# Optimization experiments

Hardware: AMD Instinct MI355X
Metric: run time of the kernel (lower is better)

Reference implementation:

```python
import jax, jax.numpy as jnp
import numpy as np
from jax import lax

BN_EPS = 1e-5

def _tern(w):
    # TWN-style ternarization with straight-through estimator
    d = 0.7 * jnp.mean(jnp.abs(w))
    q = jnp.where(jnp.abs(w) > d, jnp.sign(w), jnp.zeros_like(w))
    return w + lax.stop_gradient(q - w)

def _conv(x, w, b):
    y = lax.conv_general_dilated(x, _tern(w), (1, 1), 'SAME',
                                 dimension_numbers=('NCHW', 'OIHW', 'NCHW'))
    return y + b[None, :, None, None]

def _bn4(x, g, b, m, v):
    inv = g * lax.rsqrt(v + BN_EPS)
    return (x - m[None, :, None, None]) * inv[None, :, None, None] + b[None, :, None, None]

def _bn2(x, g, b, m, v):
    return (x - m) * (g * lax.rsqrt(v + BN_EPS)) + b

def _pool(x):
    return lax.reduce_window(x, -jnp.inf, lax.max, (1, 1, 2, 2), (1, 1, 2, 2), 'VALID')


def setup_inputs() -> dict:
    key = jax.random.key(0)
    ks = jax.random.split(key, 8)
    f = jnp.float32
    d = {}
    d['x'] = jax.random.normal(ks[0], (1024, 1, 28, 28), f)
    wshapes = {'w1': (32, 1, 3, 3), 'w2': (64, 32, 3, 3), 'w3': (128, 64, 3, 3),
               'w4': (128, 128, 3, 3), 'wf1': (256, 6272), 'wf2': (128, 256), 'wf3': (10, 128)}
    for i, (n, s) in enumerate(wshapes.items()):
        d[n] = jax.random.normal(ks[i + 1], s, f) * 0.1
    for n, c in [('1', 32), ('2', 64), ('3', 128), ('4', 128)]:
        d['b' + n] = jnp.zeros((c,), f)
        d['g' + n] = jnp.ones((c,), f)
        d['be' + n] = jnp.zeros((c,), f)
        d['m' + n] = jnp.zeros((c,), f)
        d['v' + n] = jnp.ones((c,), f)
    for n, c in [('f1', 256), ('f2', 128)]:
        d['b' + n] = jnp.zeros((c,), f)
        d['g' + n] = jnp.ones((c,), f)
        d['be' + n] = jnp.zeros((c,), f)
        d['m' + n] = jnp.zeros((c,), f)
        d['v' + n] = jnp.ones((c,), f)
    d['bf3'] = jnp.zeros((10,), f)
    return d


def reference(x, w1, b1, g1, be1, m1, v1, w2, b2, g2, be2, m2, v2,
              w3, b3, g3, be3, m3, v3, w4, b4, g4, be4, m4, v4,
              wf1, bf1, gf1, bef1, mf1, vf1, wf2, bf2, gf2, bef2, mf2, vf2,
              wf3, bf3):
    h = jax.nn.relu(_bn4(_conv(x, w1, b1), g1, be1, m1, v1))
    h = jax.nn.relu(_bn4(_conv(h, w2, b2), g2, be2, m2, v2))
    h = _pool(h)                                  # [B,64,14,14]
    h = jax.nn.relu(_bn4(_conv(h, w3, b3), g3, be3, m3, v3))
    h = jax.nn.relu(_bn4(_conv(h, w4, b4), g4, be4, m4, v4))
    h = _pool(h)                                  # [B,128,7,7]
    h = h.reshape(h.shape[0], -1)                 # [B,6272]
    h = jax.nn.relu(_bn2(h @ _tern(wf1).T + bf1, gf1, bef1, mf1, vf1))
    h = jax.nn.relu(_bn2(h @ _tern(wf2).T + bf2, gf2, bef2, mf2, vf2))
    return h @ _tern(wf3).T + bf3                 # [B,10] logits
```

## Files before the change

kernel.cpp:

```cpp
#include <hip/hip_runtime.h>
#include <hip/hip_bf16.h>

#define BN_EPS 1e-5f

typedef __attribute__((ext_vector_type(8))) short bf16x8;
typedef __attribute__((ext_vector_type(4))) float f32x4;
typedef unsigned short u16;
typedef unsigned int u32;

__device__ __forceinline__ void load16(const void* g, void* l) {
    __builtin_amdgcn_global_load_lds((const __attribute__((address_space(1))) void*)g,
                                     (__attribute__((address_space(3))) void*)l, 16, 0, 0);
}
__device__ __forceinline__ u16 f2b(float v) {
    __hip_bfloat16 h = __float2bfloat16(v);
    return *reinterpret_cast<u16*>(&h);
}
__device__ __forceinline__ float ternq(float x, float d) {
    return (fabsf(x) > d) ? (x > 0.f ? 1.f : -1.f) : 0.f;
}

constexpr size_t ALGN(size_t x) { return (x + 255) & ~(size_t)255; }
constexpr size_t O_SUMS = 0;
constexpr size_t O_W1R  = 256;
constexpr size_t O_WF2Q = ALGN(O_W1R + 288 * 4);
constexpr size_t O_WF3Q = ALGN(O_WF2Q + 32768 * 4);
constexpr size_t O_BQ2  = ALGN(O_WF3Q + 1280 * 4);
constexpr size_t O_BQ3  = ALGN(O_BQ2 + 64 * 288 * 2);
constexpr size_t O_BQ4  = ALGN(O_BQ3 + 128 * 576 * 2);
constexpr size_t O_BQF1 = ALGN(O_BQ4 + 128 * 1152 * 2);
constexpr size_t O_F1   = ALGN(O_BQF1 + (size_t)256 * 6272 * 2);
constexpr size_t O_F2   = ALGN(O_F1 + 1024 * 256 * 4);
constexpr size_t O_ACT1 = ALGN(O_F2 + 1024 * 128 * 4);
constexpr size_t O_ACT2 = ALGN(O_ACT1 + (size_t)1024 * 900 * 32 * 2);
constexpr size_t O_ACT3 = ALGN(O_ACT2 + (size_t)1024 * 256 * 64 * 2);
constexpr size_t O_ACT4 = ALGN(O_ACT3 + (size_t)1024 * 256 * 128 * 2);

__global__ void zero_sums(float* s) { if (threadIdx.x < 8) s[threadIdx.x] = 0.f; }

__device__ void absmean_seg(const float* __restrict__ w, int n4, float* __restrict__ sum,
                            int b0, int nb) {
    __shared__ float sm[256];
    float s = 0.f;
    for (int i = b0 * 256 + threadIdx.x; i < n4; i += nb * 256) {
        float4 v = ((const float4*)w)[i];
        s += fabsf(v.x) + fabsf(v.y) + fabsf(v.z) + fabsf(v.w);
    }
    sm[threadIdx.x] = s;
    __syncthreads();
    for (int o = 128; o > 0; o >>= 1) {
        if (threadIdx.x < o) sm[threadIdx.x] += sm[threadIdx.x + o];
        __syncthreads();
    }
    if (threadIdx.x == 0) atomicAdd(sum, sm[0]);
}

__global__ void absmean_all(const float* w1, const float* w2, const float* w3, const float* w4,
                            const float* wf1, const float* wf2, const float* wf3, float* sums) {
    int b = blockIdx.x;
    if (b < 160)      absmean_seg(wf1, 401408, sums + 4, b, 160);
    else if (b < 192) absmean_seg(w4, 36864, sums + 3, b - 160, 32);
    else if (b < 208) absmean_seg(w3, 18432, sums + 2, b - 192, 16);
    else if (b < 216) absmean_seg(w2, 4608, sums + 1, b - 208, 8);
    else if (b < 224) absmean_seg(wf2, 8192, sums + 5, b - 216, 8);
    else if (b < 225) absmean_seg(w1, 72, sums + 0, 0, 1);
    else              absmean_seg(wf3, 320, sums + 6, 0, 1);
}

__device__ void tern_conv_seg(const float* __restrict__ w, float d, u16* __restrict__ bq,
                              int COUT, int CIN, int b0, int nb) {
    int N = COUT * CIN * 9;
    for (int i = b0 * 256 + threadIdx.x; i < N; i += nb * 256) {
        float q = ternq(w[i], d);
        int co = i / (CIN * 9), r = i % (CIN * 9);
        int ci = r / 9, tap = r % 9;
        bq[(size_t)co * CIN * 9 + tap * CIN + ci] = f2b(q);
    }
}
__device__ void tern_f32_seg(const float* __restrict__ w, float d, float* __restrict__ wq,
                             int N, int b0, int nb) {
    for (int i = b0 * 256 + threadIdx.x; i < N; i += nb * 256) wq[i] = ternq(w[i], d);
}

__global__ void tern_all(const float* w1, const float* w2, const float* w3, const float* w4,
                         const float* wf1, const float* wf2, const float* wf3,
                         const float* __restrict__ sums,
                         float* w1r, u16* bq2, u16* bq3, u16* bq4, u16* bqf1,
                         float* wf2q, float* wf3q) {
    int b = blockIdx.x;
    if (b < 1) {
        tern_f32_seg(w1, 0.7f * sums[0] / 288.f, w1r, 288, 0, 1);
    } else if (b < 9) {
        tern_conv_seg(w2, 0.7f * sums[1] / 18432.f, bq2, 64, 32, b - 1, 8);
    } else if (b < 41) {
        tern_conv_seg(w3, 0.7f * sums[2] / 73728.f, bq3, 128, 64, b - 9, 32);
    } else if (b < 105) {
        tern_conv_seg(w4, 0.7f * sums[3] / 147456.f, bq4, 128, 128, b - 41, 64);
    } else if (b < 617) {
        float d = 0.7f * sums[4] / 1605632.f;
        for (int i = (b - 105) * 256 + threadIdx.x; i < 1605632; i += 512 * 256) {
            float q = ternq(wf1[i], d);
            int j = i / 6272, k = i % 6272;
            int c = k / 49, s = k % 49;
            bqf1[(size_t)j * 6272 + s * 128 + c] = f2b(q);
        }
    } else if (b < 633) {
        tern_f32_seg(wf2, 0.7f * sums[5] / 32768.f, wf2q, 32768, b - 617, 16);
    } else {
        tern_f32_seg(wf3, 0.7f * sums[6] / 1280.f, wf3q, 1280, 0, 1);
    }
}

__global__ void zero_f1(float* f1) {
    ((float4*)f1)[blockIdx.x * 256 + threadIdx.x] = make_float4(0.f, 0.f, 0.f, 0.f);
}

__global__ __launch_bounds__(256)
void conv1_direct(const float* __restrict__ x, const float* __restrict__ w1r,
                  const float* __restrict__ bias, const float* __restrict__ gam,
                  const float* __restrict__ bet, const float* __restrict__ mu,
                  const float* __restrict__ var, u16* __restrict__ out) {
    __shared__ float xs[784];
    __shared__ float wsh[288];
    __shared__ float scl[32], sft[32];
    const int n = blockIdx.x, tid = threadIdx.x;
    for (int i = tid; i < 784; i += 256) xs[i] = x[(size_t)n * 784 + i];
    for (int i = tid; i < 288; i += 256) wsh[i] = w1r[i];
    if (tid < 32) {
        float s = gam[tid] * rsqrtf(var[tid] + BN_EPS);
        scl[tid] = s;
        sft[tid] = (bias[tid] - mu[tid]) * s + bet[tid];
    }
    __syncthreads();
    for (int p = tid; p < 784; p += 256) {
        int y = p / 28, xx = p % 28;
        float patch[9];
#pragma unroll
        for (int dy = 0; dy < 3; ++dy)
#pragma unroll
            for (int dx = 0; dx < 3; ++dx) {
                int gy = y + dy - 1, gx = xx + dx - 1;
                patch[dy * 3 + dx] = (gy >= 0 && gy < 28 && gx >= 0 && gx < 28) ? xs[gy * 28 + gx] : 0.f;
            }
        u32 pk[16];
#pragma unroll
        for (int co = 0; co < 32; co += 2) {
            float s0 = 0.f, s1 = 0.f;
#pragma unroll
            for (int t = 0; t < 9; ++t) {
                s0 += wsh[co * 9 + t] * patch[t];
                s1 += wsh[(co + 1) * 9 + t] * patch[t];
            }
            float v0 = fmaxf(s0 * scl[co] + sft[co], 0.f);
            float v1 = fmaxf(s1 * scl[co + 1] + sft[co + 1], 0.f);
            pk[co >> 1] = ((u32)f2b(v1) << 16) | (u32)f2b(v0);
        }
        size_t base = ((size_t)(n * 30 + y + 1) * 30 + (xx + 1)) * 32;
#pragma unroll
        for (int q = 0; q < 4; ++q) ((uint4*)(out + base))[q] = ((uint4*)pk)[q];
    }
}

template<int C, int HP, int HV>
__global__ void border_zero(u16* __restrict__ buf) {
    constexpr int NB = 2 * HP + 2 * HV;
    constexpr int CG = C / 8;
    int i = blockIdx.x * blockDim.x + threadIdx.x;
    if (i >= 1024 * NB * CG) return;
    int cg = i % CG, r = i / CG;
    int b = r % NB, n = r / NB;
    int py, px;
    if (b < HP)               { py = 0;                  px = b; }
    else if (b < 2 * HP)      { py = HP - 1;             px = b - HP; }
    else if (b < 2 * HP + HV) { py = b - 2 * HP + 1;     px = 0; }
    else                      { py = b - 2 * HP - HV + 1; px = HP - 1; }
    size_t off = ((size_t)(n * HP + py) * HP + px) * C + cg * 8;
    *(uint4*)(buf + off) = make_uint4(0, 0, 0, 0);
}

template<int CIN, int BN, int HV, int HP, int G, bool POOL, bool PADOUT>
__global__ __launch_bounds__(256)
void convgemm(const u16* __restrict__ act, const u16* __restrict__ bq,
              const float* __restrict__ bias, const float* __restrict__ gam,
              const float* __restrict__ bet, const float* __restrict__ mu,
              const float* __restrict__ var, u16* __restrict__ out) {
    constexpr int BM = 128;
    constexpr int K = 9 * CIN;
    constexpr int S = K / (32 * G);
    constexpr int TPC = CIN / 32;
    constexpr int NT = BN / 32;
    constexpr int RB = BN / 64;
    constexpr int HO = HV / 2;
    constexpr int PP = POOL ? HO * HO : HV * HV;

    __shared__ __align__(16) u16 Alds[G][BM * 32];
    __shared__ __align__(16) u16 Blds[G][BN * 32];
    __shared__ int rowA[BM];
    __shared__ int rowO[BM];
    __shared__ float scl[BN], sft[BN];

    const int tid = threadIdx.x;
    const int m0 = blockIdx.x * BM;

    for (int t = tid; t < BM; t += 256) {
        int base;
        if (POOL) {
            int p = (m0 >> 2) + (t >> 2), q = t & 3;
            int n = p / PP, rr = p % PP;
            int oy = rr / HO, ox = rr % HO;
            int y = oy * 2 + (q >> 1), x = ox * 2 + (q & 1);
            base = ((n * HP + y) * HP + x) * CIN;
        } else {
            int m = m0 + t;
            int n = m / PP, rr = m % PP;
            int y = rr / HV, x = rr % HV;
            base = ((n * HP + y) * HP + x) * CIN;
        }
        rowA[t] = base;
    }
    if (POOL) {
        if (tid < 32) {
            int p = (m0 >> 2) + tid;
            int n = p / PP, rr = p % PP;
            int oy = rr / HO, ox = rr % HO;
            rowO[tid] = PADOUT ? ((n * 16 + oy + 1) * 16 + ox + 1) * BN : p * BN;
        }
    } else {
        for (int t = tid; t < BM; t += 256) {
            int m = m0 + t;
            int n = m / PP, rr = m % PP;
            int y = rr / HV, x = rr % HV;
            rowO[t] = PADOUT ? ((n * 16 + y + 1) * 16 + x + 1) * BN : m * BN;
        }
    }
    if (tid < BN) {
        float s = gam[tid] * rsqrtf(var[tid] + BN_EPS);
        scl[tid] = s;
        sft[tid] = (bias[tid] - mu[tid]) * s + bet[tid];
    }
    __syncthreads();

    int arow[2];
    arow[0] = rowA[(tid >> 6) * 16 + (tid & 15)];
    arow[1] = rowA[64 + (tid >> 6) * 16 + (tid & 15)];
    const int chunkb = ((tid >> 4) & 3) * 16;
    const int bco = (tid >> 6) * 16 + (tid & 15);
    const char* actb = (const char*)act;
    const char* bqb  = (const char*)bq;

    const int wave = tid >> 6, lane = tid & 63;
    const int wm = wave & 1, wn = wave >> 1;
    const int fr16 = lane * 16;

    f32x4 acc[4][NT] = {};

    for (int s = 0; s < S; ++s) {
#pragma unroll
        for (int j = 0; j < G; ++j) {
            int g = s * G + j;
            int tap = g / TPC, cio = (g % TPC) * 32;
            int dy = tap / 3, dx = tap % 3;
            int toffb = ((dy * HP + dx) * CIN + cio) * 2;
            char* Al = (char*)Alds[j];
#pragma unroll
            for (int r = 0; r < 2; ++r)
                load16(actb + (size_t)arow[r] * 2 + toffb + chunkb, Al + r * 4096 + tid * 16);
            char* Bl = (char*)Blds[j];
            int bkob = g * 64 + chunkb;
#pragma unroll
            for (int r = 0; r < RB; ++r)
                load16(bqb + (size_t)(r * 64 + bco) * K * 2 + bkob, Bl + r * 4096 + tid * 16);
        }
        __syncthreads();
#pragma unroll
        for (int j = 0; j < G; ++j) {
            const char* Al = (const char*)Alds[j];
            const char* Bl = (const char*)Blds[j];
            bf16x8 af[4], bf[NT];
#pragma unroll
            for (int mt = 0; mt < 4; ++mt)
                af[mt] = *(const bf16x8*)(Al + (wm * 4 + mt) * 1024 + fr16);
#pragma unroll
            for (int nt = 0; nt < NT; ++nt)
                bf[nt] = *(const bf16x8*)(Bl + (wn * NT + nt) * 1024 + fr16);
#pragma unroll
            for (int mt = 0; mt < 4; ++mt)
#pragma unroll
                for (int nt = 0; nt < NT; ++nt)
                    acc[mt][nt] = __builtin_amdgcn_mfma_f32_16x16x32_bf16(af[mt], bf[nt], acc[mt][nt], 0, 0, 0);
        }
        __syncthreads();
    }

    const int fr = lane & 15, quad = lane >> 4;
    if (POOL) {
#pragma unroll
        for (int mt = 0; mt < 4; ++mt) {
            int pl = wm * 16 + mt * 4 + quad;
            int ob = rowO[pl];
#pragma unroll
            for (int nt = 0; nt < NT; ++nt) {
                int col = wn * (NT * 16) + nt * 16 + fr;
                float sc = scl[col], sh = sft[col];
                f32x4 a = acc[mt][nt];
                float v0 = a[0] * sc + sh, v1 = a[1] * sc + sh;
                float v2 = a[2] * sc + sh, v3 = a[3] * sc + sh;
                float mx = fmaxf(fmaxf(v0, v1), fmaxf(v2, v3));
                out[(size_t)ob + col] = f2b(fmaxf(mx, 0.f));
            }
        }
    } else {
#pragma unroll
        for (int mt = 0; mt < 4; ++mt) {
            int rb = wm * 64 + mt * 16 + quad * 4;
            int o0 = rowO[rb], o1 = rowO[rb + 1], o2 = rowO[rb + 2], o3 = rowO[rb + 3];
#pragma unroll
            for (int nt = 0; nt < NT; ++nt) {
                int col = wn * (NT * 16) + nt * 16 + fr;
                float sc = scl[col], sh = sft[col];
                f32x4 a = acc[mt][nt];
                out[(size_t)o0 + col] = f2b(fmaxf(a[0] * sc + sh, 0.f));
                out[(size_t)o1 + col] = f2b(fmaxf(a[1] * sc + sh, 0.f));
                out[(size_t)o2 + col] = f2b(fmaxf(a[2] * sc + sh, 0.f));
                out[(size_t)o3 + col] = f2b(fmaxf(a[3] * sc + sh, 0.f));
            }
        }
    }
}

__global__ __launch_bounds__(256)
void fc1gemm(const u16* __restrict__ A, const u16* __restrict__ Bq, float* __restrict__ out) {
    constexpr int K = 6272, KC = 896, S = KC / 64;
    __shared__ __align__(16) u16 Alds[2][128 * 32];
    __shared__ __align__(16) u16 Blds[2][128 * 32];
    const int tid = threadIdx.x;
    const int m0 = blockIdx.x * 128;
    const int n0 = blockIdx.y * 128;
    const int k0 = blockIdx.z * KC;
    const int chunkb = ((tid >> 4) & 3) * 16;
    const int rr = (tid >> 6) * 16 + (tid & 15);
    const char* Ag = (const char*)A;
    const char* Bg = (const char*)Bq;
    const int wave = tid >> 6, lane = tid & 63;
    const int wm = wave & 1, wn = wave >> 1;
    const int fr16 = lane * 16;
    f32x4 acc[4][4] = {};

    for (int s = 0; s < S; ++s) {
#pragma unroll
        for (int j = 0; j < 2; ++j) {
            int kb = (k0 + s * 64 + j * 32) * 2 + chunkb;
            char* Al = (char*)Alds[j];
            char* Bl = (char*)Blds[j];
#pragma unroll
            for (int r = 0; r < 2; ++r) {
                load16(Ag + (size_t)(m0 + r * 64 + rr) * K * 2 + kb, Al + r * 4096 + tid * 16);
                load16(Bg + (size_t)(n0 + r * 64 + rr) * K * 2 + kb, Bl + r * 4096 + tid * 16);
            }
        }
        __syncthreads();
#pragma unroll
        for (int j = 0; j < 2; ++j) {
            const char* Al = (const char*)Alds[j];
            const char* Bl = (const char*)Blds[j];
            bf16x8 af[4], bf[4];
#pragma unroll
            for (int mt = 0; mt < 4; ++mt)
                af[mt] = *(const bf16x8*)(Al + (wm * 4 + mt) * 1024 + fr16);
#pragma unroll
            for (int nt = 0; nt < 4; ++nt)
                bf[nt] = *(const bf16x8*)(Bl + (wn * 4 + nt) * 1024 + fr16);
#pragma unroll
            for (int mt = 0; mt < 4; ++mt)
#pragma unroll
                for (int nt = 0; nt < 4; ++nt)
                    acc[mt][nt] = __builtin_amdgcn_mfma_f32_16x16x32_bf16(af[mt], bf[nt], acc[mt][nt], 0, 0, 0);
        }
        __syncthreads();
    }
    const int fr = lane & 15, quad = lane >> 4;
#pragma unroll
    for (int mt = 0; mt < 4; ++mt) {
        int row = m0 + wm * 64 + mt * 16 + quad * 4;
#pragma unroll
        for (int nt = 0; nt < 4; ++nt) {
            int col = n0 + wn * 64 + nt * 16 + fr;
            f32x4 a = acc[mt][nt];
            atomicAdd(&out[(size_t)(row + 0) * 256 + col], a[0]);
            atomicAdd(&out[(size_t)(row + 1) * 256 + col], a[1]);
            atomicAdd(&out[(size_t)(row + 2) * 256 + col], a[2]);
            atomicAdd(&out[(size_t)(row + 3) * 256 + col], a[3]);
        }
    }
}

__global__ __launch_bounds__(256)
void fc2_kernel(const float* __restrict__ A, const float* __restrict__ Bw,
                const float* __restrict__ bA, const float* __restrict__ gA,
                const float* __restrict__ beA, const float* __restrict__ mA,
                const float* __restrict__ vA,
                const float* __restrict__ bias, const float* __restrict__ gam,
                const float* __restrict__ bet, const float* __restrict__ mu,
                const float* __restrict__ var, float* __restrict__ out) {
    constexpr int M = 1024, Nn = 128, K = 256;
    __shared__ __align__(16) float As[16][68];
    __shared__ __align__(16) float Bs[16][68];
    __shared__ float sclA[256], sftA[256];
    const int tid = threadIdx.x;
    const int n0 = blockIdx.x * 64, m0 = blockIdx.y * 64;
    if (tid < 256) {
        float s = gA[tid] * rsqrtf(vA[tid] + BN_EPS);
        sclA[tid] = s;
        sftA[tid] = (bA[tid] - mA[tid]) * s + beA[tid];
    }
    const int tm = tid >> 4, tn = tid & 15;
    const int lr = tid >> 2, lk = (tid & 3) * 4;
    float acc[4][4] = {};
    __syncthreads();
    for (int k0 = 0; k0 < K; k0 += 16) {
        float4 av = *(const float4*)&A[(size_t)(m0 + lr) * K + k0 + lk];
        float4 bv = *(const float4*)&Bw[(size_t)(n0 + lr) * K + k0 + lk];
        As[lk + 0][lr] = fmaxf(av.x * sclA[k0 + lk + 0] + sftA[k0 + lk + 0], 0.f);
        As[lk + 1][lr] = fmaxf(av.y * sclA[k0 + lk + 1] + sftA[k0 + lk + 1], 0.f);
        As[lk + 2][lr] = fmaxf(av.z * sclA[k0 + lk + 2] + sftA[k0 + lk + 2], 0.f);
        As[lk + 3][lr] = fmaxf(av.w * sclA[k0 + lk + 3] + sftA[k0 + lk + 3], 0.f);
        Bs[lk + 0][lr] = bv.x; Bs[lk + 1][lr] = bv.y; Bs[lk + 2][lr] = bv.z; Bs[lk + 3][lr] = bv.w;
        __syncthreads();
#pragma unroll
        for (int k = 0; k < 16; ++k) {
            float4 a = *(const float4*)&As[k][tm * 4];
            float4 b = *(const float4*)&Bs[k][tn * 4];
            acc[0][0] += a.x * b.x; acc[0][1] += a.x * b.y; acc[0][2] += a.x * b.z; acc[0][3] += a.x * b.w;
            acc[1][0] += a.y * b.x; acc[1][1] += a.y * b.y; acc[1][2] += a.y * b.z; acc[1][3] += a.y * b.w;
            acc[2][0] += a.z * b.x; acc[2][1] += a.z * b.y; acc[2][2] += a.z * b.z; acc[2][3] += a.z * b.w;
            acc[3][0] += a.w * b.x; acc[3][1] += a.w * b.y; acc[3][2] += a.w * b.z; acc[3][3] += a.w * b.w;
        }
        __syncthreads();
    }
#pragma unroll
    for (int i = 0; i < 4; ++i) {
        int row = m0 + tm * 4 + i;
#pragma unroll
        for (int j = 0; j < 4; ++j) {
            int col = n0 + tn * 4 + j;
            float sc = gam[col] * rsqrtf(var[col] + BN_EPS);
            float v = (acc[i][j] + bias[col] - mu[col]) * sc + bet[col];
            out[(size_t)row * Nn + col] = fmaxf(v, 0.f);
        }
    }
}

__global__ __launch_bounds__(256)
void fc3_kernel(const float* __restrict__ A, const float* __restrict__ Bw,
                const float* __restrict__ bias, float* __restrict__ out) {
    int i = blockIdx.x * blockDim.x + threadIdx.x;
    if (i >= 1024 * 10) return;
    int n = i / 10, j = i % 10;
    const float4* a = (const float4*)&A[(size_t)n * 128];
    const float4* b = (const float4*)&Bw[(size_t)j * 128];
    float s = 0.f;
#pragma unroll
    for (int k = 0; k < 32; ++k) {
        float4 x = a[k], y = b[k];
        s += x.x * y.x + x.y * y.y + x.z * y.z + x.w * y.w;
    }
    out[i] = s + bias[j];
}

extern "C" void kernel_launch(void* const* d_in, const int* in_sizes, int n_in,
                              void* d_out, int out_size, void* d_ws, size_t ws_size,
                              hipStream_t stream) {
    (void)in_sizes; (void)n_in; (void)out_size; (void)ws_size;
    const float* x   = (const float*)d_in[0];
    const float* w1  = (const float*)d_in[1];
    const float* w2  = (const float*)d_in[2];
    const float* w3  = (const float*)d_in[3];
    const float* w4  = (const float*)d_in[4];
    const float* wf1 = (const float*)d_in[5];
    const float* wf2 = (const float*)d_in[6];
    const float* wf3 = (const float*)d_in[7];
    auto P = [&](int i) { return (const float*)d_in[i]; };
    char* wsb = (char*)d_ws;
    float* sums = (float*)(wsb + O_SUMS);
    float* w1r  = (float*)(wsb + O_W1R);
    float* wf2q = (float*)(wsb + O_WF2Q);
    float* wf3q = (float*)(wsb + O_WF3Q);
    u16* bq2   = (u16*)(wsb + O_BQ2);
    u16* bq3   = (u16*)(wsb + O_BQ3);
    u16* bq4   = (u16*)(wsb + O_BQ4);
    u16* bqf1  = (u16*)(wsb + O_BQF1);
    float* f1  = (float*)(wsb + O_F1);
    float* f2  = (float*)(wsb + O_F2);
    u16* act1  = (u16*)(wsb + O_ACT1);
    u16* act2p = (u16*)(wsb + O_ACT2);
    u16* act3  = (u16*)(wsb + O_ACT3);
    u16* act4p = (u16*)(wsb + O_ACT4);

    zero_sums<<<1, 64, 0, stream>>>(sums);
    absmean_all<<<226, 256, 0, stream>>>(w1, w2, w3, w4, wf1, wf2, wf3, sums);
    tern_all<<<634, 256, 0, stream>>>(w1, w2, w3, w4, wf1, wf2, wf3, sums,
                                      w1r, bq2, bq3, bq4, bqf1, wf2q, wf3q);

    border_zero<32, 30, 28><<<(1024 * 116 * 4 + 255) / 256, 256, 0, stream>>>(act1);
    border_zero<64, 16, 14><<<(1024 * 60 * 8 + 255) / 256, 256, 0, stream>>>(act2p);
    border_zero<128, 16, 14><<<(1024 * 60 * 16 + 255) / 256, 256, 0, stream>>>(act3);
    zero_f1<<<256, 256, 0, stream>>>(f1);

    conv1_direct<<<1024, 256, 0, stream>>>(x, w1r, P(8), P(9), P(10), P(11), P(12), act1);
    convgemm<32, 64, 28, 30, 3, true, true><<<6272, 256, 0, stream>>>(
        act1, bq2, P(13), P(14), P(15), P(16), P(17), act2p);
    convgemm<64, 128, 14, 16, 2, false, true><<<1568, 256, 0, stream>>>(
        act2p, bq3, P(18), P(19), P(20), P(21), P(22), act3);
    convgemm<128, 128, 14, 16, 2, true, false><<<1568, 256, 0, stream>>>(
        act3, bq4, P(23), P(24), P(25), P(26), P(27), act4p);
    fc1gemm<<<dim3(8, 2, 7), 256, 0, stream>>>(act4p, bqf1, f1);
    fc2_kernel<<<dim3(2, 16), 256, 0, stream>>>(
        f1, wf2q, P(28), P(29), P(30), P(31), P(32),
        P(33), P(34), P(35), P(36), P(37), f2);
    fc3_kernel<<<40, 256, 0, stream>>>(f2, wf3q, P(38), (float*)d_out);
}
```

Baseline: 499.7 us.

## Double-buffer LDS tiles in conv and fc1 GEMMs to overlap loads with MFMA

Replaces the load-G-slices-then-compute loop in convgemm and fc1gemm with a two-buffer pipeline. The next 32-wide K slice is prefetched into the alternate LDS buffer while MFMAs run on the current one, with one barrier per step instead of two. The aim is to hide global-to-LDS latency behind compute and to cut LDS footprint for the G=3 conv instance. In exchange there are more barriers per unit of K, and each stage issues fewer loads, so less memory traffic is in flight at once.

```diff
diff --git a/kernel.cpp b/kernel.cpp
--- a/kernel.cpp
+++ b/kernel.cpp
@@ -178,7 +178,7 @@
     *(uint4*)(buf + off) = make_uint4(0, 0, 0, 0);
 }
 
-template<int CIN, int BN, int HV, int HP, int G, bool POOL, bool PADOUT>
+template<int CIN, int BN, int HV, int HP, bool POOL, bool PADOUT>
 __global__ __launch_bounds__(256)
 void convgemm(const u16* __restrict__ act, const u16* __restrict__ bq,
               const float* __restrict__ bias, const float* __restrict__ gam,
@@ -186,15 +186,15 @@
               const float* __restrict__ var, u16* __restrict__ out) {
     constexpr int BM = 128;
     constexpr int K = 9 * CIN;
-    constexpr int S = K / (32 * G);
+    constexpr int S = K / 32;
     constexpr int TPC = CIN / 32;
     constexpr int NT = BN / 32;
     constexpr int RB = BN / 64;
     constexpr int HO = HV / 2;
     constexpr int PP = POOL ? HO * HO : HV * HV;
 
-    __shared__ __align__(16) u16 Alds[G][BM * 32];
-    __shared__ __align__(16) u16 Blds[G][BN * 32];
+    __shared__ __align__(16) u16 Alds[2][BM * 32];
+    __shared__ __align__(16) u16 Blds[2][BN * 32];
     __shared__ int rowA[BM];
     __shared__ int rowO[BM];
     __shared__ float scl[BN], sft[BN];
@@ -252,44 +252,41 @@
     const int wm = wave & 1, wn = wave >> 1;
     const int fr16 = lane * 16;
 
+    auto stage = [&](int g, int buf) {
+        int tap = g / TPC, cio = (g % TPC) * 32;
+        int dy = tap / 3, dx = tap % 3;
+        int toffb = ((dy * HP + dx) * CIN + cio) * 2;
+        char* Al = (char*)Alds[buf];
+#pragma unroll
+        for (int r = 0; r < 2; ++r)
+            load16(actb + (size_t)arow[r] * 2 + toffb + chunkb, Al + r * 4096 + tid * 16);
+        char* Bl = (char*)Blds[buf];
+        int bkob = g * 64 + chunkb;
+#pragma unroll
+        for (int r = 0; r < RB; ++r)
+            load16(bqb + (size_t)(r * 64 + bco) * K * 2 + bkob, Bl + r * 4096 + tid * 16);
+    };
+
     f32x4 acc[4][NT] = {};
-
+    stage(0, 0);
+#pragma unroll 2
     for (int s = 0; s < S; ++s) {
-#pragma unroll
-        for (int j = 0; j < G; ++j) {
-            int g = s * G + j;
-            int tap = g / TPC, cio = (g % TPC) * 32;
-            int dy = tap / 3, dx = tap % 3;
-            int toffb = ((dy * HP + dx) * CIN + cio) * 2;
-            char* Al = (char*)Alds[j];
-#pragma unroll
-            for (int r = 0; r < 2; ++r)
-                load16(actb + (size_t)arow[r] * 2 + toffb + chunkb, Al + r * 4096 + tid * 16);
-            char* Bl = (char*)Blds[j];
-            int bkob = g * 64 + chunkb;
-#pragma unroll
-            for (int r = 0; r < RB; ++r)
-                load16(bqb + (size_t)(r * 64 + bco) * K * 2 + bkob, Bl + r * 4096 + tid * 16);
-        }
         __syncthreads();
-#pragma unroll
-        for (int j = 0; j < G; ++j) {
-            const char* Al = (const char*)Alds[j];
-            const char* Bl = (const char*)Blds[j];
-            bf16x8 af[4], bf[NT];
-#pragma unroll
-            for (int mt = 0; mt < 4; ++mt)
-                af[mt] = *(const bf16x8*)(Al + (wm * 4 + mt) * 1024 + fr16);
+        if (s + 1 < S) stage(s + 1, (s + 1) & 1);
+        const char* Al = (const char*)Alds[s & 1];
+        const char* Bl = (const char*)Blds[s & 1];
+        bf16x8 af[4], bf[NT];
+#pragma unroll
+        for (int mt = 0; mt < 4; ++mt)
+            af[mt] = *(const bf16x8*)(Al + (wm * 4 + mt) * 1024 + fr16);
+#pragma unroll
+        for (int nt = 0; nt < NT; ++nt)
+            bf[nt] = *(const bf16x8*)(Bl + (wn * NT + nt) * 1024 + fr16);
+#pragma unroll
+        for (int mt = 0; mt < 4; ++mt)
 #pragma unroll
             for (int nt = 0; nt < NT; ++nt)
-                bf[nt] = *(const bf16x8*)(Bl + (wn * NT + nt) * 1024 + fr16);
-#pragma unroll
-            for (int mt = 0; mt < 4; ++mt)
-#pragma unroll
-                for (int nt = 0; nt < NT; ++nt)
-                    acc[mt][nt] = __builtin_amdgcn_mfma_f32_16x16x32_bf16(af[mt], bf[nt], acc[mt][nt], 0, 0, 0);
-        }
-        __syncthreads();
+                acc[mt][nt] = __builtin_amdgcn_mfma_f32_16x16x32_bf16(af[mt], bf[nt], acc[mt][nt], 0, 0, 0);
     }
 
     const int fr = lane & 15, quad = lane >> 4;
@@ -330,7 +327,7 @@
 
 __global__ __launch_bounds__(256)
 void fc1gemm(const u16* __restrict__ A, const u16* __restrict__ Bq, float* __restrict__ out) {
-    constexpr int K = 6272, KC = 896, S = KC / 64;
+    constexpr int K = 6272, KC = 896, S = KC / 32;
     __shared__ __align__(16) u16 Alds[2][128 * 32];
     __shared__ __align__(16) u16 Blds[2][128 * 32];
     const int tid = threadIdx.x;
@@ -346,37 +343,36 @@
     const int fr16 = lane * 16;
     f32x4 acc[4][4] = {};
 
+    auto stage = [&](int g, int buf) {
+        int kb = (k0 + g * 32) * 2 + chunkb;
+        char* Al = (char*)Alds[buf];
+        char* Bl = (char*)Blds[buf];
+#pragma unroll
+        for (int r = 0; r < 2; ++r) {
+            load16(Ag + (size_t)(m0 + r * 64 + rr) * K * 2 + kb, Al + r * 4096 + tid * 16);
+            load16(Bg + (size_t)(n0 + r * 64 + rr) * K * 2 + kb, Bl + r * 4096 + tid * 16);
+        }
+    };
+
+    stage(0, 0);
+#pragma unroll 2
     for (int s = 0; s < S; ++s) {
-#pragma unroll
-        for (int j = 0; j < 2; ++j) {
-            int kb = (k0 + s * 64 + j * 32) * 2 + chunkb;
-            char* Al = (char*)Alds[j];
-            char* Bl = (char*)Blds[j];
-#pragma unroll
-            for (int r = 0; r < 2; ++r) {
-                load16(Ag + (size_t)(m0 + r * 64 + rr) * K * 2 + kb, Al + r * 4096 + tid * 16);
-                load16(Bg + (size_t)(n0 + r * 64 + rr) * K * 2 + kb, Bl + r * 4096 + tid * 16);
-            }
-        }
         __syncthreads();
-#pragma unroll
-        for (int j = 0; j < 2; ++j) {
-            const char* Al = (const char*)Alds[j];
-            const char* Bl = (const char*)Blds[j];
-            bf16x8 af[4], bf[4];
-#pragma unroll
-            for (int mt = 0; mt < 4; ++mt)
-                af[mt] = *(const bf16x8*)(Al + (wm * 4 + mt) * 1024 + fr16);
+        if (s + 1 < S) stage(s + 1, (s + 1) & 1);
+        const char* Al = (const char*)Alds[s & 1];
+        const char* Bl = (const char*)Blds[s & 1];
+        bf16x8 af[4], bf[4];
+#pragma unroll
+        for (int mt = 0; mt < 4; ++mt)
+            af[mt] = *(const bf16x8*)(Al + (wm * 4 + mt) * 1024 + fr16);
+#pragma unroll
+        for (int nt = 0; nt < 4; ++nt)
+            bf[nt] = *(const bf16x8*)(Bl + (wn * 4 + nt) * 1024 + fr16);
+#pragma unroll
+        for (int mt = 0; mt < 4; ++mt)
 #pragma unroll
             for (int nt = 0; nt < 4; ++nt)
-                bf[nt] = *(const bf16x8*)(Bl + (wn * 4 + nt) * 1024 + fr16);
-#pragma unroll
-            for (int mt = 0; mt < 4; ++mt)
-#pragma unroll
-                for (int nt = 0; nt < 4; ++nt)
-                    acc[mt][nt] = __builtin_amdgcn_mfma_f32_16x16x32_bf16(af[mt], bf[nt], acc[mt][nt], 0, 0, 0);
-        }
-        __syncthreads();
+                acc[mt][nt] = __builtin_amdgcn_mfma_f32_16x16x32_bf16(af[mt], bf[nt], acc[mt][nt], 0, 0, 0);
     }
     const int fr = lane & 15, quad = lane >> 4;
 #pragma unroll
@@ -402,7 +398,7 @@
                 const float* __restrict__ bias, const float* __restrict__ gam,
                 const float* __restrict__ bet, const float* __restrict__ mu,
                 const float* __restrict__ var, float* __restrict__ out) {
-    constexpr int M = 1024, Nn = 128, K = 256;
+    constexpr int Nn = 128, K = 256;
     __shared__ __align__(16) float As[16][68];
     __shared__ __align__(16) float Bs[16][68];
     __shared__ float sclA[256], sftA[256];
@@ -507,11 +503,11 @@
     zero_f1<<<256, 256, 0, stream>>>(f1);
 
     conv1_direct<<<1024, 256, 0, stream>>>(x, w1r, P(8), P(9), P(10), P(11), P(12), act1);
-    convgemm<32, 64, 28, 30, 3, true, true><<<6272, 256, 0, stream>>>(
+    convgemm<32, 64, 28, 30, true, true><<<6272, 256, 0, stream>>>(
         act1, bq2, P(13), P(14), P(15), P(16), P(17), act2p);
-    convgemm<64, 128, 14, 16, 2, false, true><<<1568, 256, 0, stream>>>(
+    convgemm<64, 128, 14, 16, false, true><<<1568, 256, 0, stream>>>(
         act2p, bq3, P(18), P(19), P(20), P(21), P(22), act3);
-    convgemm<128, 128, 14, 16, 2, true, false><<<1568, 256, 0, stream>>>(
+    convgemm<128, 128, 14, 16, true, false><<<1568, 256, 0, stream>>>(
         act3, bq4, P(23), P(24), P(25), P(26), P(27), act4p);
     fc1gemm<<<dim3(8, 2, 7), 256, 0, stream>>>(act4p, bqf1, f1);
     fc2_kernel<<<dim3(2, 16), 256, 0, stream>>>(
```

Result: slower. 514.6 us (+3.0%).

## Restructure conv GEMM to 2-wave blocks with B fragments read directly from global

Applied to the files above, without the earlier changes.

The conv implicit-GEMM kernel moves from 4 waves with A and B both staged in LDS across G k-groups to 2 waves of 128 threads. Each wave now covers 64 rows and the full N width, and only A is staged in LDS, one 32-wide k-step at a time. B (ternary weight) fragments are loaded straight from global/L2 into registers, and output row offsets are recomputed in the epilogue instead of being kept in LDS. The goal is to cut LDS traffic and usage and to drop the B staging. In exchange it adds more per-wave accumulator registers (NT up to 8) and a barrier on every k-step, which lowers overlap.

```diff
diff --git a/kernel.cpp b/kernel.cpp
--- a/kernel.cpp
+++ b/kernel.cpp
@@ -178,31 +178,28 @@
     *(uint4*)(buf + off) = make_uint4(0, 0, 0, 0);
 }
 
-template<int CIN, int BN, int HV, int HP, int G, bool POOL, bool PADOUT>
-__global__ __launch_bounds__(256)
+template<int CIN, int BN, int HV, int HP, bool POOL, bool PADOUT>
+__global__ __launch_bounds__(128)
 void convgemm(const u16* __restrict__ act, const u16* __restrict__ bq,
               const float* __restrict__ bias, const float* __restrict__ gam,
               const float* __restrict__ bet, const float* __restrict__ mu,
               const float* __restrict__ var, u16* __restrict__ out) {
     constexpr int BM = 128;
     constexpr int K = 9 * CIN;
-    constexpr int S = K / (32 * G);
+    constexpr int S = K / 32;
     constexpr int TPC = CIN / 32;
-    constexpr int NT = BN / 32;
-    constexpr int RB = BN / 64;
+    constexpr int NT = BN / 16;
     constexpr int HO = HV / 2;
     constexpr int PP = POOL ? HO * HO : HV * HV;
 
-    __shared__ __align__(16) u16 Alds[G][BM * 32];
-    __shared__ __align__(16) u16 Blds[G][BN * 32];
+    __shared__ __align__(16) u16 Alds[BM * 32];
     __shared__ int rowA[BM];
-    __shared__ int rowO[BM];
     __shared__ float scl[BN], sft[BN];
 
     const int tid = threadIdx.x;
     const int m0 = blockIdx.x * BM;
 
-    for (int t = tid; t < BM; t += 256) {
+    for (int t = tid; t < BM; t += 128) {
         int base;
         if (POOL) {
             int p = (m0 >> 2) + (t >> 2), q = t & 3;
@@ -218,89 +215,68 @@
         }
         rowA[t] = base;
     }
+    for (int t = tid; t < BN; t += 128) {
+        float s = gam[t] * rsqrtf(var[t] + BN_EPS);
+        scl[t] = s;
+        sft[t] = (bias[t] - mu[t]) * s + bet[t];
+    }
+    __syncthreads();
+
+    int ab[4];
+#pragma unroll
+    for (int r = 0; r < 4; ++r) ab[r] = rowA[r * 32 + (tid >> 2)];
+    const int chunkb = (tid & 3) * 16;
+    const char* actb = (const char*)act;
+    const char* bqb  = (const char*)bq;
+    char* AB = (char*)Alds;
+
+    const int wv = tid >> 6, lane = tid & 63;
+    const int fr = lane & 15, quad = lane >> 4;
+    const int kb = quad * 16;
+
+    const char* bp[NT];
+#pragma unroll
+    for (int nt = 0; nt < NT; ++nt)
+        bp[nt] = bqb + (size_t)(nt * 16 + fr) * K * 2 + kb;
+
+    f32x4 acc[4][NT] = {};
+
+#pragma unroll 2
+    for (int s = 0; s < S; ++s) {
+        int tap = s / TPC, cio = (s % TPC) * 32;
+        int dy = tap / 3, dx = tap % 3;
+        int toffb = ((dy * HP + dx) * CIN + cio) * 2;
+#pragma unroll
+        for (int r = 0; r < 4; ++r)
+            load16(actb + (size_t)ab[r] * 2 + toffb + chunkb, AB + r * 2048 + tid * 16);
+        __syncthreads();
+
+        int boff = s * 64;
+        bf16x8 af[4], bf[NT];
+#pragma unroll
+        for (int mt = 0; mt < 4; ++mt)
+            af[mt] = *(const bf16x8*)(AB + (wv * 64 + mt * 16 + fr) * 64 + kb);
+#pragma unroll
+        for (int nt = 0; nt < NT; ++nt)
+            bf[nt] = *(const bf16x8*)(bp[nt] + boff);
+#pragma unroll
+        for (int mt = 0; mt < 4; ++mt)
+#pragma unroll
+            for (int nt = 0; nt < NT; ++nt)
+                acc[mt][nt] = __builtin_amdgcn_mfma_f32_16x16x32_bf16(af[mt], bf[nt], acc[mt][nt], 0, 0, 0);
+        __syncthreads();
+    }
+
     if (POOL) {
-        if (tid < 32) {
-            int p = (m0 >> 2) + tid;
+#pragma unroll
+        for (int mt = 0; mt < 4; ++mt) {
+            int p = (m0 >> 2) + wv * 16 + mt * 4 + quad;
             int n = p / PP, rr = p % PP;
             int oy = rr / HO, ox = rr % HO;
-            rowO[tid] = PADOUT ? ((n * 16 + oy + 1) * 16 + ox + 1) * BN : p * BN;
-        }
-    } else {
-        for (int t = tid; t < BM; t += 256) {
-            int m = m0 + t;
-            int n = m / PP, rr = m % PP;
-            int y = rr / HV, x = rr % HV;
-            rowO[t] = PADOUT ? ((n * 16 + y + 1) * 16 + x + 1) * BN : m * BN;
-        }
-    }
-    if (tid < BN) {
-        float s = gam[tid] * rsqrtf(var[tid] + BN_EPS);
-        scl[tid] = s;
-        sft[tid] = (bias[tid] - mu[tid]) * s + bet[tid];
-    }
-    __syncthreads();
-
-    int arow[2];
-    arow[0] = rowA[(tid >> 6) * 16 + (tid & 15)];
-    arow[1] = rowA[64 + (tid >> 6) * 16 + (tid & 15)];
-    const int chunkb = ((tid >> 4) & 3) * 16;
-    const int bco = (tid >> 6) * 16 + (tid & 15);
-    const char* actb = (const char*)act;
-    const char* bqb  = (const char*)bq;
-
-    const int wave = tid >> 6, lane = tid & 63;
-    const int wm = wave & 1, wn = wave >> 1;
-    const int fr16 = lane * 16;
-
-    f32x4 acc[4][NT] = {};
-
-    for (int s = 0; s < S; ++s) {
-#pragma unroll
-        for (int j = 0; j < G; ++j) {
-            int g = s * G + j;
-            int tap = g / TPC, cio = (g % TPC) * 32;
-            int dy = tap / 3, dx = tap % 3;
-            int toffb = ((dy * HP + dx) * CIN + cio) * 2;
-            char* Al = (char*)Alds[j];
-#pragma unroll
-            for (int r = 0; r < 2; ++r)
-                load16(actb + (size_t)arow[r] * 2 + toffb + chunkb, Al + r * 4096 + tid * 16);
-            char* Bl = (char*)Blds[j];
-            int bkob = g * 64 + chunkb;
-#pragma unroll
-            for (int r = 0; r < RB; ++r)
-                load16(bqb + (size_t)(r * 64 + bco) * K * 2 + bkob, Bl + r * 4096 + tid * 16);
-        }
-        __syncthreads();
-#pragma unroll
-        for (int j = 0; j < G; ++j) {
-            const char* Al = (const char*)Alds[j];
-            const char* Bl = (const char*)Blds[j];
-            bf16x8 af[4], bf[NT];
-#pragma unroll
-            for (int mt = 0; mt < 4; ++mt)
-                af[mt] = *(const bf16x8*)(Al + (wm * 4 + mt) * 1024 + fr16);
-#pragma unroll
-            for (int nt = 0; nt < NT; ++nt)
-                bf[nt] = *(const bf16x8*)(Bl + (wn * NT + nt) * 1024 + fr16);
-#pragma unroll
-            for (int mt = 0; mt < 4; ++mt)
-#pragma unroll
-                for (int nt = 0; nt < NT; ++nt)
-                    acc[mt][nt] = __builtin_amdgcn_mfma_f32_16x16x32_bf16(af[mt], bf[nt], acc[mt][nt], 0, 0, 0);
-        }
-        __syncthreads();
-    }
-
-    const int fr = lane & 15, quad = lane >> 4;
-    if (POOL) {
-#pragma unroll
-        for (int mt = 0; mt < 4; ++mt) {
-            int pl = wm * 16 + mt * 4 + quad;
-            int ob = rowO[pl];
+            int ob = (PADOUT ? ((n * 16 + oy + 1) * 16 + ox + 1) : p) * BN;
 #pragma unroll
             for (int nt = 0; nt < NT; ++nt) {
-                int col = wn * (NT * 16) + nt * 16 + fr;
+                int col = nt * 16 + fr;
                 float sc = scl[col], sh = sft[col];
                 f32x4 a = acc[mt][nt];
                 float v0 = a[0] * sc + sh, v1 = a[1] * sc + sh;
@@ -312,17 +288,23 @@
     } else {
 #pragma unroll
         for (int mt = 0; mt < 4; ++mt) {
-            int rb = wm * 64 + mt * 16 + quad * 4;
-            int o0 = rowO[rb], o1 = rowO[rb + 1], o2 = rowO[rb + 2], o3 = rowO[rb + 3];
+            int ob[4];
+#pragma unroll
+            for (int j = 0; j < 4; ++j) {
+                int m = m0 + wv * 64 + mt * 16 + quad * 4 + j;
+                int n = m / PP, rr = m % PP;
+                int y = rr / HV, x = rr % HV;
+                ob[j] = (PADOUT ? ((n * 16 + y + 1) * 16 + x + 1) : m) * BN;
+            }
 #pragma unroll
             for (int nt = 0; nt < NT; ++nt) {
-                int col = wn * (NT * 16) + nt * 16 + fr;
+                int col = nt * 16 + fr;
                 float sc = scl[col], sh = sft[col];
                 f32x4 a = acc[mt][nt];
-                out[(size_t)o0 + col] = f2b(fmaxf(a[0] * sc + sh, 0.f));
-                out[(size_t)o1 + col] = f2b(fmaxf(a[1] * sc + sh, 0.f));
-                out[(size_t)o2 + col] = f2b(fmaxf(a[2] * sc + sh, 0.f));
-                out[(size_t)o3 + col] = f2b(fmaxf(a[3] * sc + sh, 0.f));
+                out[(size_t)ob[0] + col] = f2b(fmaxf(a[0] * sc + sh, 0.f));
+                out[(size_t)ob[1] + col] = f2b(fmaxf(a[1] * sc + sh, 0.f));
+                out[(size_t)ob[2] + col] = f2b(fmaxf(a[2] * sc + sh, 0.f));
+                out[(size_t)ob[3] + col] = f2b(fmaxf(a[3] * sc + sh, 0.f));
             }
         }
     }
@@ -402,7 +384,7 @@
                 const float* __restrict__ bias, const float* __restrict__ gam,
                 const float* __restrict__ bet, const float* __restrict__ mu,
                 const float* __restrict__ var, float* __restrict__ out) {
-    constexpr int M = 1024, Nn = 128, K = 256;
+    constexpr int Nn = 128, K = 256;
     __shared__ __align__(16) float As[16][68];
     __shared__ __align__(16) float Bs[16][68];
     __shared__ float sclA[256], sftA[256];
@@ -507,11 +489,11 @@
     zero_f1<<<256, 256, 0, stream>>>(f1);
 
     conv1_direct<<<1024, 256, 0, stream>>>(x, w1r, P(8), P(9), P(10), P(11), P(12), act1);
-    convgemm<32, 64, 28, 30, 3, true, true><<<6272, 256, 0, stream>>>(
+    convgemm<32, 64, 28, 30, true, true><<<6272, 128, 0, stream>>>(
         act1, bq2, P(13), P(14), P(15), P(16), P(17), act2p);
-    convgemm<64, 128, 14, 16, 2, false, true><<<1568, 256, 0, stream>>>(
+    convgemm<64, 128, 14, 16, false, true><<<1568, 128, 0, stream>>>(
         act2p, bq3, P(18), P(19), P(20), P(21), P(22), act3);
-    convgemm<128, 128, 14, 16, 2, true, false><<<1568, 256, 0, stream>>>(
+    convgemm<128, 128, 14, 16, true, false><<<1568, 128, 0, stream>>>(
         act3, bq4, P(23), P(24), P(25), P(26), P(27), act4p);
     fc1gemm<<<dim3(8, 2, 7), 256, 0, stream>>>(act4p, bqf1, f1);
     fc2_kernel<<<dim3(2, 16), 256, 0, stream>>>(
```

Result: slower. 591.0 us (+18.3%).

## Fuse conv3 and conv4 into one per-image LDS-resident MFMA kernel

Applied to the files above, without the earlier changes.

Replaces the two separate convgemm launches for conv3 and conv4 with a single kernel that processes one image per block. The block keeps the padded conv2 output in swizzled LDS, computes conv3 with MFMA, writes its BN+ReLU result back into LDS with a zeroed border, then computes conv4 plus BN, ReLU and 2x2 pooling. Weights for conv3 and conv4 are ternarized straight into a fragment-ready layout so each lane reads B operands directly from global memory. This removes the act3 global round-trip and its border-zero pass. It also changes a template parameter of the conv2 convgemm launch. The cost is heavy register use (two 7x4 accumulator arrays) and 64KB of LDS per block, which may limit occupancy.

```diff
diff --git a/kernel.cpp b/kernel.cpp
--- a/kernel.cpp
+++ b/kernel.cpp
@@ -77,6 +77,19 @@
         bq[(size_t)co * CIN * 9 + tap * CIN + ci] = f2b(q);
     }
 }
+__device__ void tern_conv_prime_seg(const float* __restrict__ w, float d, u16* __restrict__ bqp,
+                                    int CIN, int b0, int nb) {
+    int N = 128 * CIN * 9;
+    for (int i = b0 * 256 + threadIdx.x; i < N; i += nb * 256) {
+        float q = ternq(w[i], d);
+        int co = i / (CIN * 9), r = i % (CIN * 9);
+        int ci = r / 9, tap = r % 9;
+        int k = tap * CIN + ci;
+        int s = k >> 5, qd = (k & 31) >> 3, e = k & 7;
+        int lane = qd * 16 + (co & 15), nt = co >> 4;
+        bqp[((size_t)(s * 8 + nt) * 64 + lane) * 8 + e] = f2b(q);
+    }
+}
 __device__ void tern_f32_seg(const float* __restrict__ w, float d, float* __restrict__ wq,
                              int N, int b0, int nb) {
     for (int i = b0 * 256 + threadIdx.x; i < N; i += nb * 256) wq[i] = ternq(w[i], d);
@@ -85,7 +98,7 @@
 __global__ void tern_all(const float* w1, const float* w2, const float* w3, const float* w4,
                          const float* wf1, const float* wf2, const float* wf3,
                          const float* __restrict__ sums,
-                         float* w1r, u16* bq2, u16* bq3, u16* bq4, u16* bqf1,
+                         float* w1r, u16* bq2, u16* bq3p, u16* bq4p, u16* bqf1,
                          float* wf2q, float* wf3q) {
     int b = blockIdx.x;
     if (b < 1) {
@@ -93,9 +106,9 @@
     } else if (b < 9) {
         tern_conv_seg(w2, 0.7f * sums[1] / 18432.f, bq2, 64, 32, b - 1, 8);
     } else if (b < 41) {
-        tern_conv_seg(w3, 0.7f * sums[2] / 73728.f, bq3, 128, 64, b - 9, 32);
+        tern_conv_prime_seg(w3, 0.7f * sums[2] / 73728.f, bq3p, 64, b - 9, 32);
     } else if (b < 105) {
-        tern_conv_seg(w4, 0.7f * sums[3] / 147456.f, bq4, 128, 128, b - 41, 64);
+        tern_conv_prime_seg(w4, 0.7f * sums[3] / 147456.f, bq4p, 128, b - 41, 64);
     } else if (b < 617) {
         float d = 0.7f * sums[4] / 1605632.f;
         for (int i = (b - 105) * 256 + threadIdx.x; i < 1605632; i += 512 * 256) {
@@ -323,6 +336,152 @@
                 out[(size_t)o1 + col] = f2b(fmaxf(a[1] * sc + sh, 0.f));
                 out[(size_t)o2 + col] = f2b(fmaxf(a[2] * sc + sh, 0.f));
                 out[(size_t)o3 + col] = f2b(fmaxf(a[3] * sc + sh, 0.f));
+            }
+        }
+    }
+}
+
+__global__ __launch_bounds__(256)
+void conv34(const u16* __restrict__ act2p, const u16* __restrict__ b3p, const u16* __restrict__ b4p,
+            const float* __restrict__ b3, const float* __restrict__ g3, const float* __restrict__ be3,
+            const float* __restrict__ m3, const float* __restrict__ v3,
+            const float* __restrict__ b4, const float* __restrict__ g4, const float* __restrict__ be4,
+            const float* __restrict__ m4, const float* __restrict__ v4,
+            u16* __restrict__ out) {
+    __shared__ __align__(16) u16 Xs[32768];
+
+    const int tid = threadIdx.x;
+    const int n = blockIdx.x;
+    const int wave = tid >> 6, lane = tid & 63;
+    const int wm = wave & 1, wn = wave >> 1;
+    const int fr = lane & 15, quad = lane >> 4;
+    char* X = (char*)Xs;
+
+    float scl3[4], sft3[4], scl4[4], sft4[4];
+#pragma unroll
+    for (int nt = 0; nt < 4; ++nt) {
+        int c = wn * 64 + nt * 16 + fr;
+        float s = g3[c] * rsqrtf(v3[c] + BN_EPS);
+        scl3[nt] = s; sft3[nt] = (b3[c] - m3[c]) * s + be3[c];
+        s = g4[c] * rsqrtf(v4[c] + BN_EPS);
+        scl4[nt] = s; sft4[nt] = (b4[c] - m4[c]) * s + be4[c];
+    }
+
+    {
+        const uint4* src = (const uint4*)(act2p + (size_t)n * 16384);
+#pragma unroll
+        for (int it = 0; it < 8; ++it) {
+            int i = it * 256 + tid;
+            int r = i >> 3, c = i & 7;
+            uint4 v = src[i];
+            *(uint4*)(X + r * 128 + ((c ^ (r & 7)) * 16)) = v;
+        }
+    }
+    __syncthreads();
+
+    int r0a[7];
+#pragma unroll
+    for (int mtl = 0; mtl < 7; ++mtl) {
+        int g = wm * 7 + mtl + 1;
+        int pxc = min(max(fr, 1), 14);
+        r0a[mtl] = (g - 1) * 16 + (pxc - 1);
+    }
+    f32x4 acc[7][4] = {};
+    const char* B3 = (const char*)b3p;
+#pragma unroll 3
+    for (int s = 0; s < 18; ++s) {
+        int tap = s >> 1;
+        int rdel = (tap / 3) * 16 + tap % 3;
+        int cs = (s & 1) * 4;
+        bf16x8 af[7], bf[4];
+#pragma unroll
+        for (int mtl = 0; mtl < 7; ++mtl) {
+            int r = r0a[mtl] + rdel;
+            int pos = (cs + quad) ^ (r & 7);
+            af[mtl] = *(const bf16x8*)(X + r * 128 + pos * 16);
+        }
+#pragma unroll
+        for (int nt = 0; nt < 4; ++nt)
+            bf[nt] = *(const bf16x8*)(B3 + ((size_t)((s * 8 + wn * 4 + nt) * 64 + lane)) * 16);
+#pragma unroll
+        for (int mtl = 0; mtl < 7; ++mtl)
+#pragma unroll
+            for (int nt = 0; nt < 4; ++nt)
+                acc[mtl][nt] = __builtin_amdgcn_mfma_f32_16x16x32_bf16(af[mtl], bf[nt], acc[mtl][nt], 0, 0, 0);
+    }
+    __syncthreads();
+
+    for (int t = tid; t < 60 * 16; t += 256) {
+        int j = t & 15, b = t >> 4;
+        int m = (b < 16) ? b : (b < 32) ? 240 + (b - 16) : (b < 46) ? (b - 31) * 16 : (b - 45) * 16 + 15;
+        *(uint4*)(X + m * 256 + j * 16) = make_uint4(0, 0, 0, 0);
+    }
+#pragma unroll
+    for (int mtl = 0; mtl < 7; ++mtl) {
+        int g = wm * 7 + mtl + 1;
+#pragma unroll
+        for (int nt = 0; nt < 4; ++nt) {
+            int col = wn * 64 + nt * 16 + fr;
+            int c = col >> 3;
+            f32x4 a = acc[mtl][nt];
+#pragma unroll
+            for (int j = 0; j < 4; ++j) {
+                int px = quad * 4 + j;
+                if (px >= 1 && px <= 14) {
+                    int m = g * 16 + px;
+                    float v = fmaxf(a[j] * scl3[nt] + sft3[nt], 0.f);
+                    *(u16*)(X + m * 256 + ((c ^ (m & 15)) * 16) + (col & 7) * 2) = f2b(v);
+                }
+            }
+        }
+    }
+    __syncthreads();
+
+    int r0b[7];
+#pragma unroll
+    for (int mtl = 0; mtl < 7; ++mtl) {
+        int m = (wm * 7 + mtl) * 16 + fr;
+        int p = min(m >> 2, 48), q = m & 3;
+        int y2 = (p / 7) * 2 + (q >> 1), x2 = (p % 7) * 2 + (q & 1);
+        r0b[mtl] = y2 * 16 + x2;
+    }
+    f32x4 acc4[7][4] = {};
+    const char* B4 = (const char*)b4p;
+#pragma unroll 2
+    for (int s = 0; s < 36; ++s) {
+        int tap = s >> 2;
+        int rdel = (tap / 3) * 16 + tap % 3;
+        int cs = (s & 3) * 4;
+        bf16x8 af[7], bf[4];
+#pragma unroll
+        for (int mtl = 0; mtl < 7; ++mtl) {
+            int r = r0b[mtl] + rdel;
+            int pos = (cs + quad) ^ (r & 15);
+            af[mtl] = *(const bf16x8*)(X + r * 256 + pos * 16);
+        }
+#pragma unroll
+        for (int nt = 0; nt < 4; ++nt)
+            bf[nt] = *(const bf16x8*)(B4 + ((size_t)((s * 8 + wn * 4 + nt) * 64 + lane)) * 16);
+#pragma unroll
+        for (int mtl = 0; mtl < 7; ++mtl)
+#pragma unroll
+            for (int nt = 0; nt < 4; ++nt)
+                acc4[mtl][nt] = __builtin_amdgcn_mfma_f32_16x16x32_bf16(af[mtl], bf[nt], acc4[mtl][nt], 0, 0, 0);
+    }
+#pragma unroll
+    for (int mtl = 0; mtl < 7; ++mtl) {
+        int p = (wm * 7 + mtl) * 4 + quad;
+        if (p < 49) {
+#pragma unroll
+            for (int nt = 0; nt < 4; ++nt) {
+                int col = wn * 64 + nt * 16 + fr;
+                f32x4 a = acc4[mtl][nt];
+                float v0 = a[0] * scl4[nt] + sft4[nt];
+                float v1 = a[1] * scl4[nt] + sft4[nt];
+                float v2 = a[2] * scl4[nt] + sft4[nt];
+                float v3 = a[3] * scl4[nt] + sft4[nt];
+                float mx = fmaxf(fmaxf(v0, v1), fmaxf(v2, v3));
+                out[((size_t)n * 49 + p) * 128 + col] = f2b(fmaxf(mx, 0.f));
             }
         }
     }
@@ -402,7 +561,7 @@
                 const float* __restrict__ bias, const float* __restrict__ gam,
                 const float* __restrict__ bet, const float* __restrict__ mu,
                 const float* __restrict__ var, float* __restrict__ out) {
-    constexpr int M = 1024, Nn = 128, K = 256;
+    constexpr int Nn = 128, K = 256;
     __shared__ __align__(16) float As[16][68];
     __shared__ __align__(16) float Bs[16][68];
     __shared__ float sclA[256], sftA[256];
@@ -486,33 +645,31 @@
     float* wf2q = (float*)(wsb + O_WF2Q);
     float* wf3q = (float*)(wsb + O_WF3Q);
     u16* bq2   = (u16*)(wsb + O_BQ2);
-    u16* bq3   = (u16*)(wsb + O_BQ3);
-    u16* bq4   = (u16*)(wsb + O_BQ4);
+    u16* bq3p  = (u16*)(wsb + O_BQ3);
+    u16* bq4p  = (u16*)(wsb + O_BQ4);
     u16* bqf1  = (u16*)(wsb + O_BQF1);
     float* f1  = (float*)(wsb + O_F1);
     float* f2  = (float*)(wsb + O_F2);
     u16* act1  = (u16*)(wsb + O_ACT1);
     u16* act2p = (u16*)(wsb + O_ACT2);
-    u16* act3  = (u16*)(wsb + O_ACT3);
     u16* act4p = (u16*)(wsb + O_ACT4);
 
     zero_sums<<<1, 64, 0, stream>>>(sums);
     absmean_all<<<226, 256, 0, stream>>>(w1, w2, w3, w4, wf1, wf2, wf3, sums);
     tern_all<<<634, 256, 0, stream>>>(w1, w2, w3, w4, wf1, wf2, wf3, sums,
-                                      w1r, bq2, bq3, bq4, bqf1, wf2q, wf3q);
+                                      w1r, bq2, bq3p, bq4p, bqf1, wf2q, wf3q);
 
     border_zero<32, 30, 28><<<(1024 * 116 * 4 + 255) / 256, 256, 0, stream>>>(act1);
     border_zero<64, 16, 14><<<(1024 * 60 * 8 + 255) / 256, 256, 0, stream>>>(act2p);
-    border_zero<128, 16, 14><<<(1024 * 60 * 16 + 255) / 256, 256, 0, stream>>>(act3);
     zero_f1<<<256, 256, 0, stream>>>(f1);
 
     conv1_direct<<<1024, 256, 0, stream>>>(x, w1r, P(8), P(9), P(10), P(11), P(12), act1);
-    convgemm<32, 64, 28, 30, 3, true, true><<<6272, 256, 0, stream>>>(
+    convgemm<32, 64, 28, 30, 1, true, true><<<6272, 256, 0, stream>>>(
         act1, bq2, P(13), P(14), P(15), P(16), P(17), act2p);
-    convgemm<64, 128, 14, 16, 2, false, true><<<1568, 256, 0, stream>>>(
-        act2p, bq3, P(18), P(19), P(20), P(21), P(22), act3);
-    convgemm<128, 128, 14, 16, 2, true, false><<<1568, 256, 0, stream>>>(
-        act3, bq4, P(23), P(24), P(25), P(26), P(27), act4p);
+    conv34<<<1024, 256, 0, stream>>>(
+        act2p, bq3p, bq4p,
+        P(18), P(19), P(20), P(21), P(22),
+        P(23), P(24), P(25), P(26), P(27), act4p);
     fc1gemm<<<dim3(8, 2, 7), 256, 0, stream>>>(act4p, bqf1, f1);
     fc2_kernel<<<dim3(2, 16), 256, 0, stream>>>(
         f1, wf2q, P(28), P(29), P(30), P(31), P(32),
```

Measured after the change: 417.2 us. 1.2x faster.
